# Kernel tuning notes

Measured on AMD Instinct MI355X. Metric: run time of the kernel, lower is better.

The kernel has to match this reference:

```python
import jax, jax.numpy as jnp
import numpy as np

D = 1024
B, S = 4, 2048

def setup_inputs() -> dict:
    key = jax.random.key(0)
    ks = jax.random.split(key, 4)
    scale = 1.0 / np.sqrt(D)
    return {
        "x": jax.random.normal(ks[0], (B, S, D), dtype=jnp.float32),
        "Wq": jax.random.normal(ks[1], (D, D), dtype=jnp.float32) * scale,
        "bq": jnp.zeros((D,), jnp.float32),
        "Wk": jax.random.normal(ks[2], (D, D), dtype=jnp.float32) * scale,
        "bk": jnp.zeros((D,), jnp.float32),
        "Wv": jax.random.normal(ks[3], (D, D), dtype=jnp.float32) * scale,
        "bv": jnp.zeros((D,), jnp.float32),
    }

def reference(x, Wq, bq, Wk, bk, Wv, bv):
    # torch Linear: y = x @ W.T + b
    Q = jnp.einsum('bsd,ed->bse', x, Wq) + bq
    K = jnp.einsum('bsd,ed->bse', x, Wk) + bk
    V = jnp.einsum('bsd,ed->bse', x, Wv) + bv
    # NOTE: original scales by sqrt(K.shape[1]) == sqrt(seq_len), kept faithfully
    dk = K.shape[1]
    logits = jnp.einsum('bqd,bkd->bqk', Q, K) / jnp.sqrt(jnp.asarray(dk, Q.dtype))
    att = jax.nn.softmax(logits, axis=-1)
    return jnp.einsum('bqk,bkd->bqd', att, V)
```

## Files before the change

### kernel.cpp

```cpp
#include <hip/hip_runtime.h>


typedef unsigned short u16;
typedef unsigned int u32;
typedef __bf16 bf16x8 __attribute__((ext_vector_type(8)));
typedef float floatx4 __attribute__((ext_vector_type(4)));

__device__ __forceinline__ u16 f2bf(float f) {
    u32 u = __float_as_uint(f);
    u += 0x7fffu + ((u >> 16) & 1u);
    return (u16)(u >> 16);
}

__device__ __forceinline__ void g2lds16(const void* g, void* l) {
    __builtin_amdgcn_global_load_lds(
        (const __attribute__((address_space(1))) unsigned int*)g,
        (__attribute__((address_space(3))) unsigned int*)l,
        16, 0, 0);
}

__global__ __launch_bounds__(256)
void cvt_all(const float* __restrict__ x, const float* __restrict__ Wq,
             const float* __restrict__ Wk, const float* __restrict__ Wv,
             u16* __restrict__ xb, u16* __restrict__ wall,
             float* __restrict__ rowsum)
{
    const int NX = 2097152;
    const int NW = 262144;
    const int TOT = NX + 3 * NW;
    int i = blockIdx.x * 256 + threadIdx.x;
    if (i >= TOT) {
        int z = i - TOT;
        float4 zz = {0.f, 0.f, 0.f, 0.f};
        ((float4*)rowsum)[z] = zz;
        return;
    }
    const float* src;
    u16* dst;
    int idx;
    if (i < NX) { src = x; dst = xb; idx = i; }
    else {
        int j = i - NX;
        dst = wall; idx = j;
        src = (j < NW) ? Wq : (j < 2 * NW) ? Wk : Wv;
        int jj = (j < NW) ? j : (j < 2 * NW) ? (j - NW) : (j - 2 * NW);
        float4 v = ((const float4*)src)[jj];
        ushort4 o;
        o.x = f2bf(v.x); o.y = f2bf(v.y); o.z = f2bf(v.z); o.w = f2bf(v.w);
        ((ushort4*)dst)[idx] = o;
        return;
    }
    float4 v = ((const float4*)src)[idx];
    ushort4 o;
    o.x = f2bf(v.x); o.y = f2bf(v.y); o.z = f2bf(v.z); o.w = f2bf(v.w);
    ((ushort4*)dst)[idx] = o;
}

template<int MODE>
__global__ __launch_bounds__(256)
void gemm_bt(const u16* __restrict__ A, const u16* __restrict__ B,
             void* __restrict__ Out, const float* __restrict__ bias,
             float scale, int M, int N, int K,
             long long sAz, long long sBz, long long sOz,
             void* __restrict__ Out2, void* __restrict__ Out3,
             const float* __restrict__ bias2, const float* __restrict__ bias3,
             float* __restrict__ rowsum)
{
    __shared__ u16 ldsA[2][128 * 64];
    __shared__ u16 ldsB[2][128 * 64];

    const int tid   = threadIdx.x;
    const int lane  = tid & 63;
    const int wv    = tid >> 6;
    const int wm    = (wv >> 1) * 64;
    const int wn    = (wv & 1) * 64;
    const int lhalf = lane & 15;
    const int quad  = lane >> 4;

    const size_t bz = blockIdx.z;
    A += bz * (size_t)sAz;
    B += bz * (size_t)sBz;

    int tm, tn;
    {
        const int ntn = gridDim.x, ntm = gridDim.y;
        const int lin = blockIdx.y * ntn + blockIdx.x;
        const int GM = 4;
        const int width = GM * ntn;
        const int group = lin / width;
        const int first = group * GM;
        const int gsz   = (ntm - first) < GM ? (ntm - first) : GM;
        const int rem   = lin - group * width;
        tm = first + rem % gsz;
        tn = rem / gsz;
    }
    const int m0 = tm * 128;
    const int n0 = tn * 128;

    const int r8 = lane >> 3;
    const int gc = (lane & 7) ^ r8;
    const u16* pa = A + (size_t)(m0 + wv * 32 + r8) * K + gc * 8;
    const u16* pb = B + (size_t)(n0 + wv * 32 + r8) * K + gc * 8;
    const int lofs = wv * 2048;

    floatx4 zero = {0.f, 0.f, 0.f, 0.f};
    floatx4 acc[4][4];
#pragma unroll
    for (int i = 0; i < 4; ++i)
#pragma unroll
        for (int j = 0; j < 4; ++j) acc[i][j] = zero;

    const int swz = lhalf & 7;

#pragma unroll
    for (int j = 0; j < 4; ++j) {
        g2lds16(pa + (size_t)(j * 8) * K, &ldsA[0][lofs + j * 512]);
        g2lds16(pb + (size_t)(j * 8) * K, &ldsB[0][lofs + j * 512]);
    }
    pa += 64; pb += 64;

    int buf = 0;
    for (int k0 = 0; k0 < K; k0 += 64) {
        __syncthreads();
        if (k0 + 64 < K) {
#pragma unroll
            for (int j = 0; j < 4; ++j) {
                g2lds16(pa + (size_t)(j * 8) * K, &ldsA[buf ^ 1][lofs + j * 512]);
                g2lds16(pb + (size_t)(j * 8) * K, &ldsB[buf ^ 1][lofs + j * 512]);
            }
            pa += 64; pb += 64;
        }

        const u16* lA = ldsA[buf];
        const u16* lB = ldsB[buf];
#pragma unroll
        for (int ks = 0; ks < 2; ++ks) {
            const int c = ks * 4 + quad;
            const int p = c ^ swz;
            bf16x8 af[4], bfv[4];
#pragma unroll
            for (int i = 0; i < 4; ++i)
                af[i] = *(const bf16x8*)(lA + (wm + i * 16 + lhalf) * 64 + p * 8);
#pragma unroll
            for (int j = 0; j < 4; ++j)
                bfv[j] = *(const bf16x8*)(lB + (wn + j * 16 + lhalf) * 64 + p * 8);
#pragma unroll
            for (int i = 0; i < 4; ++i)
#pragma unroll
                for (int j = 0; j < 4; ++j)
                    acc[i][j] = __builtin_amdgcn_mfma_f32_16x16x32_bf16(
                        af[i], bfv[j], acc[i][j], 0, 0, 0);
        }
        buf ^= 1;
    }

#pragma unroll
    for (int i = 0; i < 4; ++i) {
        const int mb = m0 + wm + i * 16 + quad * 4;
        if (MODE == 3) {
#pragma unroll
            for (int j = 0; j < 4; ++j) {
                const int n = n0 + wn + j * 16 + lhalf;
                if (n < 1024) {
                    const float bb = bias[n];
#pragma unroll
                    for (int r = 0; r < 4; ++r)
                        ((u16*)Out)[(size_t)(mb + r) * 1024 + n] =
                            f2bf(acc[i][j][r] + bb);
                } else if (n < 2048) {
                    const float bb = bias2[n - 1024];
#pragma unroll
                    for (int r = 0; r < 4; ++r)
                        ((u16*)Out2)[(size_t)(mb + r) * 1024 + (n - 1024)] =
                            f2bf(acc[i][j][r] + bb);
                } else {
                    const int d = n - 2048;
                    const float bb = bias3[d];
                    const int b = mb >> 11;
                    const int s0 = mb & 2047;
                    ushort4 w;
                    w.x = f2bf(acc[i][j][0] + bb);
                    w.y = f2bf(acc[i][j][1] + bb);
                    w.z = f2bf(acc[i][j][2] + bb);
                    w.w = f2bf(acc[i][j][3] + bb);
                    *(ushort4*)((u16*)Out3 + (size_t)b * 2097152 +
                                (size_t)d * 2048 + s0) = w;
                }
            }
        } else if (MODE == 4) {
#pragma unroll
            for (int r = 0; r < 4; ++r) {
                const int m = mb + r;
                float rs = 0.f;
#pragma unroll
                for (int j = 0; j < 4; ++j) {
                    const int n = n0 + wn + j * 16 + lhalf;
                    const float e = __expf(acc[i][j][r] * scale);
                    ((u16*)Out)[bz * (size_t)sOz + (size_t)m * N + n] = f2bf(e);
                    rs += e;
                }
                rs += __shfl_xor(rs, 1, 64);
                rs += __shfl_xor(rs, 2, 64);
                rs += __shfl_xor(rs, 4, 64);
                rs += __shfl_xor(rs, 8, 64);
                if (lhalf == 0)
                    atomicAdd(&rowsum[bz * 2048 + m], rs);
            }
        } else {
            float4 rs4 = *(const float4*)&rowsum[bz * 2048 + mb];
            float rinv[4];
            rinv[0] = __builtin_amdgcn_rcpf(rs4.x);
            rinv[1] = __builtin_amdgcn_rcpf(rs4.y);
            rinv[2] = __builtin_amdgcn_rcpf(rs4.z);
            rinv[3] = __builtin_amdgcn_rcpf(rs4.w);
#pragma unroll
            for (int j = 0; j < 4; ++j) {
                const int n = n0 + wn + j * 16 + lhalf;
#pragma unroll
                for (int r = 0; r < 4; ++r)
                    ((float*)Out)[bz * (size_t)sOz + (size_t)(mb + r) * N + n] =
                        acc[i][j][r] * rinv[r];
            }
        }
    }
}

template<int MODE>
__global__ __launch_bounds__(512, 2)
void gemm8p(const u16* __restrict__ A, const u16* __restrict__ B,
            void* __restrict__ Out, const float* __restrict__ bias,
            float scale, int M, int N, int K,
            long long sAz, long long sBz, long long sOz,
            void* __restrict__ Out2, void* __restrict__ Out3,
            const float* __restrict__ bias2, const float* __restrict__ bias3,
            float* __restrict__ rowsum)
{
    __shared__ u16 lds[2][2][2][8192];

    const int tid   = threadIdx.x;
    const int lane  = tid & 63;
    const int wv    = tid >> 6;
    const int wr    = wv >> 2;
    const int wc    = wv & 3;
    const int lhalf = lane & 15;
    const int quad  = lane >> 4;
    const int swz   = lhalf & 7;

    const size_t bz = blockIdx.z;
    A += bz * (size_t)sAz;
    B += bz * (size_t)sBz;

    int tm, tn;
    {
        const int ntn = gridDim.x, ntm = gridDim.y;
        const int lin = blockIdx.y * ntn + blockIdx.x;
        const int GM = 4;
        const int width = GM * ntn;
        const int group = lin / width;
        const int first = group * GM;
        const int gsz   = (ntm - first) < GM ? (ntm - first) : GM;
        const int rem   = lin - group * width;
        tm = first + rem % gsz;
        tn = rem / gsz;
    }
    const int m0 = tm * 256;
    const int n0 = tn * 256;

    const int r8l = lane >> 3;
    const int gc  = (lane & 7) ^ r8l;
    const u16* pA = A + (size_t)(m0 + wv * 8 + r8l) * K + gc * 8;
    const u16* pB = B + (size_t)(n0 + wv * 8 + r8l) * K + gc * 8;
    const int wofs = wv * 512;

    const int NT = K >> 6;

#define STAGE8(op, slot, half, kt) do {                                        \
    const u16* _s = ((op) ? pB : pA) + (size_t)((half) * 128) * K              \
                    + (size_t)(kt) * 64;                                       \
    u16* _d = &lds[slot][op][half][wofs];                                      \
    g2lds16(_s, _d);                                                           \
    g2lds16(_s + (size_t)64 * K, _d + 4096);                                   \
} while (0)

    bf16x8 af[2][4];
    bf16x8 bfr[2][2][2];
    floatx4 zero = {0.f, 0.f, 0.f, 0.f};
    floatx4 acc[2][2][4][2];
#pragma unroll
    for (int a = 0; a < 2; ++a)
#pragma unroll
    for (int b = 0; b < 2; ++b)
#pragma unroll
    for (int i = 0; i < 4; ++i)
#pragma unroll
    for (int j = 0; j < 2; ++j) acc[a][b][i][j] = zero;

#define LDA8(slot, qm) do {                                                    \
    const u16* _a = &lds[slot][0][qm][0];                                      \
    _Pragma("unroll")                                                          \
    for (int ks = 0; ks < 2; ++ks) {                                           \
        const int p8 = ((ks * 4 + quad) ^ swz) * 8;                            \
        _Pragma("unroll")                                                      \
        for (int i = 0; i < 4; ++i)                                            \
            af[ks][i] = *(const bf16x8*)(_a + (wr * 64 + i * 16 + lhalf) * 64  \
                                         + p8);                                \
    }                                                                          \
} while (0)

#define LDB8(slot, qn) do {                                                    \
    const u16* _b = &lds[slot][1][qn][0];                                      \
    _Pragma("unroll")                                                          \
    for (int ks = 0; ks < 2; ++ks) {                                           \
        const int p8 = ((ks * 4 + quad) ^ swz) * 8;                            \
        _Pragma("unroll")                                                      \
        for (int j = 0; j < 2; ++j)                                            \
            bfr[qn][ks][j] = *(const bf16x8*)(_b +                             \
                (wc * 32 + j * 16 + lhalf) * 64 + p8);                         \
    }                                                                          \
} while (0)

#define MFMAQ(qm, qn) do {                                                     \
    _Pragma("unroll")                                                          \
    for (int ks = 0; ks < 2; ++ks)                                             \
        _Pragma("unroll")                                                      \
        for (int i = 0; i < 4; ++i)                                            \
            _Pragma("unroll")                                                  \
            for (int j = 0; j < 2; ++j)                                        \
                acc[qm][qn][i][j] = __builtin_amdgcn_mfma_f32_16x16x32_bf16(   \
                    af[ks][i], bfr[qn][ks][j], acc[qm][qn][i][j], 0, 0, 0);    \
} while (0)

    STAGE8(0, 0, 0, 0);
    STAGE8(1, 0, 0, 0);
    STAGE8(0, 0, 1, 0);
    STAGE8(1, 0, 1, 0);
    if (NT > 1) {
        STAGE8(0, 1, 0, 1);
        STAGE8(1, 1, 0, 1);
    }
    asm volatile("s_waitcnt vmcnt(4)");
    __builtin_amdgcn_s_barrier();

    for (int t = 0; t < NT; ++t) {
        const int s = t & 1;
        const bool p1 = (t + 1 < NT), p2 = (t + 2 < NT);

        LDA8(s, 0);
        LDB8(s, 0);
        if (p1) STAGE8(0, s ^ 1, 1, t + 1);
        __builtin_amdgcn_s_barrier();
        asm volatile("s_waitcnt lgkmcnt(0)");
        __builtin_amdgcn_s_setprio(1);
        MFMAQ(0, 0);
        __builtin_amdgcn_s_setprio(0);
        __builtin_amdgcn_s_barrier();

        LDB8(s, 1);
        if (p1) STAGE8(1, s ^ 1, 1, t + 1);
        __builtin_amdgcn_s_barrier();
        asm volatile("s_waitcnt lgkmcnt(0)");
        __builtin_amdgcn_s_setprio(1);
        MFMAQ(0, 1);
        __builtin_amdgcn_s_setprio(0);
        __builtin_amdgcn_s_barrier();

        LDA8(s, 1);
        if (p2) STAGE8(0, s, 0, t + 2);
        __builtin_amdgcn_s_barrier();
        asm volatile("s_waitcnt lgkmcnt(0)");
        __builtin_amdgcn_s_setprio(1);
        MFMAQ(1, 0);
        __builtin_amdgcn_s_setprio(0);
        __builtin_amdgcn_s_barrier();

        if (p2) STAGE8(1, s, 0, t + 2);
        __builtin_amdgcn_s_barrier();
        asm volatile("s_waitcnt lgkmcnt(0)");
        __builtin_amdgcn_s_setprio(1);
        MFMAQ(1, 1);
        __builtin_amdgcn_s_setprio(0);
        if (p2) asm volatile("s_waitcnt vmcnt(4)");
        else    asm volatile("s_waitcnt vmcnt(0)");
        __builtin_amdgcn_s_barrier();
    }

#undef STAGE8
#undef LDA8
#undef LDB8
#undef MFMAQ

#pragma unroll
    for (int qm = 0; qm < 2; ++qm)
#pragma unroll
    for (int i = 0; i < 4; ++i) {
        const int mb = m0 + qm * 128 + wr * 64 + i * 16 + quad * 4;
        if (MODE == 3) {
#pragma unroll
            for (int qn = 0; qn < 2; ++qn)
#pragma unroll
            for (int j = 0; j < 2; ++j) {
                const int n = n0 + qn * 128 + wc * 32 + j * 16 + lhalf;
                const floatx4 a = acc[qm][qn][i][j];
                if (n < 1024) {
                    const float bb = bias[n];
#pragma unroll
                    for (int r = 0; r < 4; ++r)
                        ((u16*)Out)[(size_t)(mb + r) * 1024 + n] =
                            f2bf(a[r] + bb);
                } else if (n < 2048) {
                    const float bb = bias2[n - 1024];
#pragma unroll
                    for (int r = 0; r < 4; ++r)
                        ((u16*)Out2)[(size_t)(mb + r) * 1024 + (n - 1024)] =
                            f2bf(a[r] + bb);
                } else {
                    const int d = n - 2048;
                    const float bb = bias3[d];
                    const int b = mb >> 11;
                    const int s0 = mb & 2047;
                    ushort4 w;
                    w.x = f2bf(a[0] + bb);
                    w.y = f2bf(a[1] + bb);
                    w.z = f2bf(a[2] + bb);
                    w.w = f2bf(a[3] + bb);
                    *(ushort4*)((u16*)Out3 + (size_t)b * 2097152 +
                                (size_t)d * 2048 + s0) = w;
                }
            }
        } else {
#pragma unroll
            for (int r = 0; r < 4; ++r) {
                const int m = mb + r;
                float rs = 0.f;
#pragma unroll
                for (int qn = 0; qn < 2; ++qn)
#pragma unroll
                for (int j = 0; j < 2; ++j) {
                    const int n = n0 + qn * 128 + wc * 32 + j * 16 + lhalf;
                    const float e = __expf(acc[qm][qn][i][j][r] * scale);
                    ((u16*)Out)[bz * (size_t)sOz + (size_t)m * N + n] = f2bf(e);
                    rs += e;
                }
                rs += __shfl_xor(rs, 1, 64);
                rs += __shfl_xor(rs, 2, 64);
                rs += __shfl_xor(rs, 4, 64);
                rs += __shfl_xor(rs, 8, 64);
                if (lhalf == 0)
                    atomicAdd(&rowsum[bz * 2048 + m], rs);
            }
        }
    }
}

extern "C" void kernel_launch(void* const* d_in, const int* in_sizes, int n_in,
                              void* d_out, int out_size, void* d_ws, size_t ws_size,
                              hipStream_t stream)
{
    const float* x  = (const float*)d_in[0];
    const float* Wq = (const float*)d_in[1];
    const float* bq = (const float*)d_in[2];
    const float* Wk = (const float*)d_in[3];
    const float* bk = (const float*)d_in[4];
    const float* Wv = (const float*)d_in[5];
    const float* bv = (const float*)d_in[6];
    float* out = (float*)d_out;

    const int B = 4, S = 2048, D = 1024;
    const long long SD = (long long)S * D;
    const long long SS = (long long)S * S;
    const long long BSD = (long long)B * SD;
    const long long DD = (long long)D * D;

    u16* xb   = (u16*)d_ws;
    u16* wall = xb   + BSD;
    u16* Qb   = wall + 3 * DD;
    u16* Kb   = Qb   + BSD;
    u16* Vt   = Kb   + BSD;
    u16* Sc   = Vt   + BSD;
    float* rowsum = (float*)(Sc + B * SS);

    cvt_all<<<dim3(11272), 256, 0, stream>>>(x, Wq, Wk, Wv, xb, wall, rowsum);

    gemm8p<3><<<dim3(3 * D / 256, (B * S) / 256, 1), 512, 0, stream>>>(
        xb, wall, Qb, bq, 1.f, B * S, 3 * D, D, 0, 0, 0,
        Kb, Vt, bk, bv, nullptr);

    const float sc = 0.022097086912079608f;
    gemm8p<4><<<dim3(S / 256, S / 256, B), 512, 0, stream>>>(
        Qb, Kb, Sc, nullptr, sc, S, S, D, SD, SD, SS,
        nullptr, nullptr, nullptr, nullptr, rowsum);

    gemm_bt<5><<<dim3(D / 128, S / 128, B), 256, 0, stream>>>(
        Sc, Vt, out, nullptr, 1.f, S, D, S, SS, SD, SD,
        nullptr, nullptr, nullptr, nullptr, rowsum);
}
```

Before: 255.8 us.

## Restructure GEMM main loop with register double-buffered fragments and unrolled-by-two schedule

Rewrites the 256x256 bf16 GEMM main loop to process two K-tiles per iteration. Each LDS fragment read is issued one quadrant ahead of the MFMA block that consumes it, using separate A/B fragment register sets, and quadrant order is reordered (00,01,11,10) so fragments are reused across adjacent blocks. The previous loop used two barriers plus a full lgkmcnt wait around each quadrant; the new one has one barrier per quadrant and a deeper global-to-LDS prefetch (vmcnt 6). It aims to hide LDS latency behind MFMAs and reduce synchronization, at the cost of more VGPRs and tighter correctness reliance on the manual waitcnt schedule. NT is assumed even for the paired loop.

```diff
diff --git a/kernel.cpp b/kernel.cpp
--- a/kernel.cpp
+++ b/kernel.cpp
@@ -274,52 +274,40 @@
 
     const int NT = K >> 6;
 
-#define STAGE8(op, slot, half, kt) do {                                        \
-    const u16* _s = ((op) ? pB : pA) + (size_t)((half) * 128) * K              \
+#define STG(opB, slot, half, kt) do {                                          \
+    const u16* _s = ((opB) ? pB : pA) + (size_t)((half) * 128) * K             \
                     + (size_t)(kt) * 64;                                       \
-    u16* _d = &lds[slot][op][half][wofs];                                      \
+    u16* _d = &lds[slot][opB][half][wofs];                                     \
     g2lds16(_s, _d);                                                           \
     g2lds16(_s + (size_t)64 * K, _d + 4096);                                   \
 } while (0)
 
-    bf16x8 af[2][4];
-    bf16x8 bfr[2][2][2];
-    floatx4 zero = {0.f, 0.f, 0.f, 0.f};
-    floatx4 acc[2][2][4][2];
-#pragma unroll
-    for (int a = 0; a < 2; ++a)
-#pragma unroll
-    for (int b = 0; b < 2; ++b)
-#pragma unroll
-    for (int i = 0; i < 4; ++i)
-#pragma unroll
-    for (int j = 0; j < 2; ++j) acc[a][b][i][j] = zero;
-
-#define LDA8(slot, qm) do {                                                    \
-    const u16* _a = &lds[slot][0][qm][0];                                      \
+#define LDA(dst, slot, half) do {                                              \
+    const u16* _p = &lds[slot][0][half][0];                                    \
     _Pragma("unroll")                                                          \
     for (int ks = 0; ks < 2; ++ks) {                                           \
         const int p8 = ((ks * 4 + quad) ^ swz) * 8;                            \
         _Pragma("unroll")                                                      \
         for (int i = 0; i < 4; ++i)                                            \
-            af[ks][i] = *(const bf16x8*)(_a + (wr * 64 + i * 16 + lhalf) * 64  \
-                                         + p8);                                \
+            dst[ks][i] = *(const bf16x8*)(_p + (wr * 64 + i * 16 + lhalf) * 64 \
+                                          + p8);                               \
     }                                                                          \
 } while (0)
 
-#define LDB8(slot, qn) do {                                                    \
-    const u16* _b = &lds[slot][1][qn][0];                                      \
+#define LDB(dst, slot, half) do {                                              \
+    const u16* _p = &lds[slot][1][half][0];                                    \
     _Pragma("unroll")                                                          \
     for (int ks = 0; ks < 2; ++ks) {                                           \
         const int p8 = ((ks * 4 + quad) ^ swz) * 8;                            \
         _Pragma("unroll")                                                      \
         for (int j = 0; j < 2; ++j)                                            \
-            bfr[qn][ks][j] = *(const bf16x8*)(_b +                             \
-                (wc * 32 + j * 16 + lhalf) * 64 + p8);                         \
+            dst[ks][j] = *(const bf16x8*)(_p + (wc * 32 + j * 16 + lhalf) * 64 \
+                                          + p8);                               \
     }                                                                          \
 } while (0)
 
-#define MFMAQ(qm, qn) do {                                                     \
+#define MFMAQ(qm, qn, Af, Bf) do {                                             \
+    __builtin_amdgcn_s_setprio(1);                                             \
     _Pragma("unroll")                                                          \
     for (int ks = 0; ks < 2; ++ks)                                             \
         _Pragma("unroll")                                                      \
@@ -327,67 +315,85 @@
             _Pragma("unroll")                                                  \
             for (int j = 0; j < 2; ++j)                                        \
                 acc[qm][qn][i][j] = __builtin_amdgcn_mfma_f32_16x16x32_bf16(   \
-                    af[ks][i], bfr[qn][ks][j], acc[qm][qn][i][j], 0, 0, 0);    \
+                    Af[ks][i], Bf[ks][j], acc[qm][qn][i][j], 0, 0, 0);         \
+    __builtin_amdgcn_s_setprio(0);                                             \
 } while (0)
 
-    STAGE8(0, 0, 0, 0);
-    STAGE8(1, 0, 0, 0);
-    STAGE8(0, 0, 1, 0);
-    STAGE8(1, 0, 1, 0);
+#define FENCE() do {                                                           \
+    if (full) asm volatile("s_waitcnt vmcnt(6)" ::: "memory");                 \
+    else      asm volatile("s_waitcnt vmcnt(0)" ::: "memory");                 \
+    __builtin_amdgcn_s_barrier();                                              \
+} while (0)
+
+    bf16x8 a0[2][4], a1[2][4];
+    bf16x8 b1f[2][2], b0a[2][2], b0b[2][2];
+    floatx4 zero = {0.f, 0.f, 0.f, 0.f};
+    floatx4 acc[2][2][4][2];
+#pragma unroll
+    for (int a = 0; a < 2; ++a)
+#pragma unroll
+    for (int b = 0; b < 2; ++b)
+#pragma unroll
+    for (int i = 0; i < 4; ++i)
+#pragma unroll
+    for (int j = 0; j < 2; ++j) acc[a][b][i][j] = zero;
+
+    STG(0, 0, 0, 0); STG(1, 0, 0, 0); STG(0, 0, 1, 0); STG(1, 0, 1, 0);
     if (NT > 1) {
-        STAGE8(0, 1, 0, 1);
-        STAGE8(1, 1, 0, 1);
-    }
-    asm volatile("s_waitcnt vmcnt(4)");
+        STG(0, 1, 0, 1); STG(1, 1, 0, 1); STG(0, 1, 1, 1);
+        asm volatile("s_waitcnt vmcnt(6)" ::: "memory");
+    } else {
+        asm volatile("s_waitcnt vmcnt(0)" ::: "memory");
+    }
     __builtin_amdgcn_s_barrier();
-
-    for (int t = 0; t < NT; ++t) {
-        const int s = t & 1;
-        const bool p1 = (t + 1 < NT), p2 = (t + 2 < NT);
-
-        LDA8(s, 0);
-        LDB8(s, 0);
-        if (p1) STAGE8(0, s ^ 1, 1, t + 1);
-        __builtin_amdgcn_s_barrier();
-        asm volatile("s_waitcnt lgkmcnt(0)");
-        __builtin_amdgcn_s_setprio(1);
-        MFMAQ(0, 0);
-        __builtin_amdgcn_s_setprio(0);
-        __builtin_amdgcn_s_barrier();
-
-        LDB8(s, 1);
-        if (p1) STAGE8(1, s ^ 1, 1, t + 1);
-        __builtin_amdgcn_s_barrier();
-        asm volatile("s_waitcnt lgkmcnt(0)");
-        __builtin_amdgcn_s_setprio(1);
-        MFMAQ(0, 1);
-        __builtin_amdgcn_s_setprio(0);
-        __builtin_amdgcn_s_barrier();
-
-        LDA8(s, 1);
-        if (p2) STAGE8(0, s, 0, t + 2);
-        __builtin_amdgcn_s_barrier();
-        asm volatile("s_waitcnt lgkmcnt(0)");
-        __builtin_amdgcn_s_setprio(1);
-        MFMAQ(1, 0);
-        __builtin_amdgcn_s_setprio(0);
-        __builtin_amdgcn_s_barrier();
-
-        if (p2) STAGE8(1, s, 0, t + 2);
-        __builtin_amdgcn_s_barrier();
-        asm volatile("s_waitcnt lgkmcnt(0)");
-        __builtin_amdgcn_s_setprio(1);
-        MFMAQ(1, 1);
-        __builtin_amdgcn_s_setprio(0);
-        if (p2) asm volatile("s_waitcnt vmcnt(4)");
-        else    asm volatile("s_waitcnt vmcnt(0)");
-        __builtin_amdgcn_s_barrier();
-    }
-
-#undef STAGE8
-#undef LDA8
-#undef LDB8
+    LDA(a0, 0, 0);
+    LDB(b0a, 0, 0);
+
+    for (int t = 0; t < NT; t += 2) {
+        const bool g2   = (t + 2 < NT);
+        const bool g3   = (t + 3 < NT);
+        const bool full = g3;
+
+        LDB(b1f, 0, 1);
+        if (t + 1 < NT) STG(1, 1, 1, t + 1);
+        MFMAQ(0, 0, a0, b0a);
+        FENCE();
+        LDA(a1, 0, 1);
+        if (g2) STG(0, 0, 0, t + 2);
+        MFMAQ(0, 1, a0, b1f);
+        FENCE();
+        LDA(a0, 1, 0);
+        if (g2) STG(1, 0, 0, t + 2);
+        MFMAQ(1, 1, a1, b1f);
+        FENCE();
+        LDB(b0b, 1, 0);
+        if (g2) STG(0, 0, 1, t + 2);
+        MFMAQ(1, 0, a1, b0a);
+        FENCE();
+
+        LDB(b1f, 1, 1);
+        if (g2) STG(1, 0, 1, t + 2);
+        MFMAQ(0, 0, a0, b0b);
+        FENCE();
+        LDA(a1, 1, 1);
+        if (g3) STG(0, 1, 0, t + 3);
+        MFMAQ(0, 1, a0, b1f);
+        FENCE();
+        if (g2) LDA(a0, 0, 0);
+        if (g3) STG(1, 1, 0, t + 3);
+        MFMAQ(1, 1, a1, b1f);
+        FENCE();
+        if (g2) LDB(b0a, 0, 0);
+        if (g3) STG(0, 1, 1, t + 3);
+        MFMAQ(1, 0, a1, b0b);
+        FENCE();
+    }
+
+#undef STG
+#undef LDA
+#undef LDB
 #undef MFMAQ
+#undef FENCE
 
 #pragma unroll
     for (int qm = 0; qm < 2; ++qm)
```

Result: slower. 419.0 us (+63.8%).
